# Kernel optimization log

Hardware: AMD Instinct MI355X
Metric: run time of the kernel (lower is better)

The kernel has to match this reference:

```python
import jax, jax.numpy as jnp
import numpy as np

L = 2048  # episode_len
B = 64    # batch
K = 256   # key_size
V = 256   # value_size
H = 8     # num_head


def setup_inputs() -> dict:
    key = jax.random.key(0)
    ks = jax.random.split(key, 9)
    query = jax.random.normal(ks[0], (B, K), dtype=jnp.float32)
    keys = jax.random.normal(ks[1], (L, B, K), dtype=jnp.float32)
    vals = jax.random.normal(ks[2], (L, B, V), dtype=jnp.float32)
    rpe_mod = jax.random.uniform(ks[3], (L, B, 1), dtype=jnp.float32)
    Wq = jax.random.normal(ks[4], (K, H * K), dtype=jnp.float32) * (1.0 / np.sqrt(K))
    bq = jnp.zeros((H * K,), dtype=jnp.float32)
    Wa = jax.random.normal(ks[5], (H * V, V), dtype=jnp.float32) * (1.0 / np.sqrt(H * V))
    ba = jnp.zeros((V,), dtype=jnp.float32)
    # per-sample valid length in [1, L] (nonzero so the softmax is well-defined,
    # matching read()'s early-return guard for empty memories)
    steps = jax.random.randint(ks[6], (B,), 1, L + 1, dtype=jnp.int32)
    return {"query": query, "keys": keys, "vals": vals, "rpe_mod": rpe_mod,
            "Wq": Wq, "bq": bq, "Wa": Wa, "ba": ba, "steps": steps}


def reference(query, keys, vals, rpe_mod, Wq, bq, Wa, ba, steps):
    # query encoder: [B,K] -> [B,H,K]
    q = (query @ Wq + bq).reshape(B, H, K)
    # RPE-modulated keys: [L,B,K]
    mod_keys = keys * rpe_mod
    # scores[l,b,h] = <mod_keys[l,b,:], q[b,h,:]>
    scores = jnp.einsum('lbk,bhk->lbh', mod_keys, q)
    # mask out positions >= steps[b] (equivalent to slicing keys[:step[i], i])
    valid = (jnp.arange(L, dtype=jnp.int32)[:, None] < steps[None, :])  # [L,B]
    scores = jnp.where(valid[:, :, None], scores, -jnp.inf)
    weight = jax.nn.softmax(scores, axis=0)  # softmax over stored steps
    # weighted memory read: [B,H,V]
    read = jnp.einsum('lbh,lbv->bhv', weight, vals)
    # head aggregation: [B, H*V] -> [B, V]
    out = read.reshape(B, H * V) @ Wa + ba
    return out
```

## Files before the change

### kernel.cpp

```cpp
#include <hip/hip_runtime.h>
#include <hip/hip_bf16.h>
#include <cstdint>

#define Ln 2048
#define Bn 64
#define Kd 256
#define Vd 256
#define Hn 8

#define CH 64
#define NCH 32

using u32 = unsigned int;
using u16 = unsigned short;

__device__ __forceinline__ float bflo(u32 u) { return __uint_as_float(u << 16); }
__device__ __forceinline__ float bfhi(u32 u) { return __uint_as_float(u & 0xffff0000u); }
__device__ __forceinline__ float bf1(u16 s) { return __uint_as_float(((u32)s) << 16); }
__device__ __forceinline__ float dot4(float4 a, float4 b) {
  return a.x * b.x + a.y * b.y + a.z * b.z + a.w * b.w;
}

__device__ __forceinline__ bool sniff_bf16(const void* keys) {
  const u16* q = (const u16*)keys;
  int lane = threadIdx.x & 63;
  u16 u = q[2 * (lane * 127)];
  u32 e = (u >> 7) & 0xff;
  bool sane = (u == 0) || (e >= 100 && e <= 134);
  return __popcll(__ballot(sane)) > 32;
}

__global__ __launch_bounds__(256) void k_prep(const void* keys, const void* query,
                                              const void* Wq, const void* bq,
                                              float* q_ws) {
  const bool bf = sniff_bf16(keys);
  const int t = threadIdx.x;
  const int chunk = blockIdx.x;
  const int b = blockIdx.y;

  __shared__ float ql[256];
  ql[t] = bf ? bf1(((const u16*)query)[b * 256 + t]) : ((const float*)query)[b * 256 + t];
  __syncthreads();

  int c0 = chunk * 512 + 2 * t;
  float a0, a1;
  if (bf) { a0 = bf1(((const u16*)bq)[c0]); a1 = bf1(((const u16*)bq)[c0 + 1]); }
  else    { a0 = ((const float*)bq)[c0];    a1 = ((const float*)bq)[c0 + 1]; }

  if (bf) {
    const u32* w = (const u32*)Wq + chunk * 256 + t;
    for (int k0 = 0; k0 < 256; k0 += 16) {
      u32 wv[16];
#pragma unroll
      for (int j = 0; j < 16; j++) wv[j] = w[(size_t)(k0 + j) * 1024];
#pragma unroll
      for (int j = 0; j < 16; j++) {
        float qk = ql[k0 + j];
        a0 += qk * bflo(wv[j]); a1 += qk * bfhi(wv[j]);
      }
    }
  } else {
    const float2* w = (const float2*)Wq + chunk * 256 + t;
    for (int k0 = 0; k0 < 256; k0 += 16) {
      float2 wv[16];
#pragma unroll
      for (int j = 0; j < 16; j++) wv[j] = w[(size_t)(k0 + j) * 1024];
#pragma unroll
      for (int j = 0; j < 16; j++) {
        float qk = ql[k0 + j];
        a0 += qk * wv[j].x; a1 += qk * wv[j].y;
      }
    }
  }
  q_ws[b * 2048 + c0] = a0;
  q_ws[b * 2048 + c0 + 1] = a1;
}

__global__ __launch_bounds__(256) void k_fused(const void* keys, const void* vals,
                                               const void* rpe, const int* steps,
                                               const float* q_ws, float* O_part,
                                               float2* mz_part) {
  const int b = blockIdx.y, chunk = blockIdx.x;
  const int lstart = chunk * CH;
  const int stepb = steps[b];
  if (lstart >= stepb) return;
  const int lcnt = min(CH, stepb - lstart);
  const bool bf = sniff_bf16(keys);
  const int t = threadIdx.x;
  const int lane = t & 63;
  const int wave = __builtin_amdgcn_readfirstlane(t >> 6);

  __shared__ __align__(16) float q_lds[Hn * Kd];
  __shared__ __align__(16) float w_lds[CH * 12];
  __shared__ float rpe_lds[CH];
  __shared__ float2 mz_lds[8];

  const int r8 = lane >> 3, ks8 = lane & 7;

#define LOAD_K(P, BB)                                                         \
  float4 P##0, P##1, P##2, P##3, P##4, P##5, P##6, P##7;                      \
  do {                                                                        \
    const int row_ = (BB) * 32 + wave * 8 + r8;                               \
    if (bf) {                                                                 \
      const u16* kb = (const u16*)keys +                                      \
          ((size_t)(lstart + row_) * 64 + b) * 256 + ks8 * 4;                 \
      uint2 u0 = *(const uint2*)(kb + 0);   uint2 u1 = *(const uint2*)(kb + 32);  \
      uint2 u2 = *(const uint2*)(kb + 64);  uint2 u3 = *(const uint2*)(kb + 96);  \
      uint2 u4 = *(const uint2*)(kb + 128); uint2 u5 = *(const uint2*)(kb + 160); \
      uint2 u6 = *(const uint2*)(kb + 192); uint2 u7 = *(const uint2*)(kb + 224); \
      P##0 = make_float4(bflo(u0.x), bfhi(u0.x), bflo(u0.y), bfhi(u0.y));     \
      P##1 = make_float4(bflo(u1.x), bfhi(u1.x), bflo(u1.y), bfhi(u1.y));     \
      P##2 = make_float4(bflo(u2.x), bfhi(u2.x), bflo(u2.y), bfhi(u2.y));     \
      P##3 = make_float4(bflo(u3.x), bfhi(u3.x), bflo(u3.y), bfhi(u3.y));     \
      P##4 = make_float4(bflo(u4.x), bfhi(u4.x), bflo(u4.y), bfhi(u4.y));     \
      P##5 = make_float4(bflo(u5.x), bfhi(u5.x), bflo(u5.y), bfhi(u5.y));     \
      P##6 = make_float4(bflo(u6.x), bfhi(u6.x), bflo(u6.y), bfhi(u6.y));     \
      P##7 = make_float4(bflo(u7.x), bfhi(u7.x), bflo(u7.y), bfhi(u7.y));     \
    } else {                                                                  \
      const float* kb = (const float*)keys +                                  \
          ((size_t)(lstart + row_) * 64 + b) * 256 + ks8 * 4;                 \
      P##0 = *(const float4*)(kb + 0);   P##1 = *(const float4*)(kb + 32);    \
      P##2 = *(const float4*)(kb + 64);  P##3 = *(const float4*)(kb + 96);    \
      P##4 = *(const float4*)(kb + 128); P##5 = *(const float4*)(kb + 160);   \
      P##6 = *(const float4*)(kb + 192); P##7 = *(const float4*)(kb + 224);   \
    }                                                                         \
  } while (0)

#define QF(H, J) (*(const float4*)(qp + (H) * 256 + (J) * 32))
#define SCH(P, H)                                                             \
  (dot4(P##0, QF(H, 0)) + dot4(P##1, QF(H, 1)) + dot4(P##2, QF(H, 2)) +       \
   dot4(P##3, QF(H, 3)) + dot4(P##4, QF(H, 4)) + dot4(P##5, QF(H, 5)) +       \
   dot4(P##6, QF(H, 6)) + dot4(P##7, QF(H, 7)))
#define R3(A)                                                                 \
  A += __shfl_xor(A, 1); A += __shfl_xor(A, 2); A += __shfl_xor(A, 4);

#define COMPUTE_WRITE(P, BB) do {                                             \
    const int row_ = (BB) * 32 + wave * 8 + r8;                               \
    float a0 = SCH(P, 0), a1 = SCH(P, 1), a2 = SCH(P, 2), a3 = SCH(P, 3);     \
    float a4 = SCH(P, 4), a5 = SCH(P, 5), a6 = SCH(P, 6), a7 = SCH(P, 7);     \
    R3(a0) R3(a1) R3(a2) R3(a3) R3(a4) R3(a5) R3(a6) R3(a7)                   \
    if (ks8 == 0) {                                                           \
      float rp = rpe_lds[row_];                                               \
      w_lds[row_ * 12 + 0] = a0 * rp; w_lds[row_ * 12 + 1] = a1 * rp;         \
      w_lds[row_ * 12 + 2] = a2 * rp; w_lds[row_ * 12 + 3] = a3 * rp;         \
      w_lds[row_ * 12 + 4] = a4 * rp; w_lds[row_ * 12 + 5] = a5 * rp;         \
      w_lds[row_ * 12 + 6] = a6 * rp; w_lds[row_ * 12 + 7] = a7 * rp;         \
    }                                                                         \
  } while (0)

  LOAD_K(p, 0);

  {
    const float4* src = (const float4*)(q_ws + (size_t)b * 2048) + t * 2;
    float4 f0 = src[0], f1 = src[1];
    *((float4*)q_lds + t * 2) = f0;
    *((float4*)q_lds + t * 2 + 1) = f1;
  }
  if (t < CH) {
    int l = lstart + t;
    rpe_lds[t] = bf ? bf1(((const u16*)rpe)[l * 64 + b]) : ((const float*)rpe)[l * 64 + b];
  }
  __syncthreads();

  const float* qp = q_lds + ks8 * 4;

  LOAD_K(s, 1);
  COMPUTE_WRITE(p, 0);
  COMPUTE_WRITE(s, 1);
  __syncthreads();

  {
    const int h = t >> 5, j = t & 31;
    float s0 = (j < lcnt) ? w_lds[j * 12 + h] : -3.0e38f;
    float s1 = (j + 32 < lcnt) ? w_lds[(j + 32) * 12 + h] : -3.0e38f;
    float m = fmaxf(s0, s1);
#pragma unroll
    for (int off = 16; off >= 1; off >>= 1) m = fmaxf(m, __shfl_xor(m, off, 32));
    float e0 = (j < lcnt) ? __expf(s0 - m) : 0.f;
    float e1 = (j + 32 < lcnt) ? __expf(s1 - m) : 0.f;
    w_lds[j * 12 + h] = e0;
    w_lds[(j + 32) * 12 + h] = e1;
    float zs = e0 + e1;
#pragma unroll
    for (int off = 16; off >= 1; off >>= 1) zs += __shfl_xor(zs, off, 32);
    if (j == 0) mz_lds[h] = make_float2(m, zs);
  }
  __syncthreads();
  if (t < 8) mz_part[((size_t)chunk * 64 + b) * 8 + t] = mz_lds[t];

  const int vslot = lane & 15, rg = lane >> 4;
  float acc[8][4];
#pragma unroll
  for (int hh = 0; hh < 8; hh++)
#pragma unroll
    for (int cc = 0; cc < 4; cc++) acc[hh][cc] = 0.f;

  if (bf) {
    const u32* vb = (const u32*)vals + ((size_t)lstart * 64 + b) * 128 + wave * 32 + vslot * 2;
    for (int i0 = 0; i0 < 16; i0 += 8) {
      uint2 uu[8];
#pragma unroll
      for (int jb = 0; jb < 8; jb++) {
        int row = rg + 4 * (i0 + jb);
        uu[jb] = *(const uint2*)(vb + (size_t)row * 8192);
      }
#pragma unroll
      for (int jb = 0; jb < 8; jb++) {
        int row = rg + 4 * (i0 + jb);
        float4 w0 = *(const float4*)&w_lds[row * 12];
        float4 w1 = *(const float4*)&w_lds[row * 12 + 4];
        float v0 = bflo(uu[jb].x), v1 = bfhi(uu[jb].x);
        float v2 = bflo(uu[jb].y), v3 = bfhi(uu[jb].y);
        acc[0][0] += w0.x * v0; acc[0][1] += w0.x * v1; acc[0][2] += w0.x * v2; acc[0][3] += w0.x * v3;
        acc[1][0] += w0.y * v0; acc[1][1] += w0.y * v1; acc[1][2] += w0.y * v2; acc[1][3] += w0.y * v3;
        acc[2][0] += w0.z * v0; acc[2][1] += w0.z * v1; acc[2][2] += w0.z * v2; acc[2][3] += w0.z * v3;
        acc[3][0] += w0.w * v0; acc[3][1] += w0.w * v1; acc[3][2] += w0.w * v2; acc[3][3] += w0.w * v3;
        acc[4][0] += w1.x * v0; acc[4][1] += w1.x * v1; acc[4][2] += w1.x * v2; acc[4][3] += w1.x * v3;
        acc[5][0] += w1.y * v0; acc[5][1] += w1.y * v1; acc[5][2] += w1.y * v2; acc[5][3] += w1.y * v3;
        acc[6][0] += w1.z * v0; acc[6][1] += w1.z * v1; acc[6][2] += w1.z * v2; acc[6][3] += w1.z * v3;
        acc[7][0] += w1.w * v0; acc[7][1] += w1.w * v1; acc[7][2] += w1.w * v2; acc[7][3] += w1.w * v3;
      }
    }
  } else {
    const float* vb = (const float*)vals + ((size_t)lstart * 64 + b) * 256 + wave * 64 + vslot * 4;
    for (int i0 = 0; i0 < 16; i0 += 8) {
      float4 vv[8];
#pragma unroll
      for (int jb = 0; jb < 8; jb++) {
        int row = rg + 4 * (i0 + jb);
        vv[jb] = *(const float4*)(vb + (size_t)row * 16384);
      }
#pragma unroll
      for (int jb = 0; jb < 8; jb++) {
        int row = rg + 4 * (i0 + jb);
        float4 w0 = *(const float4*)&w_lds[row * 12];
        float4 w1 = *(const float4*)&w_lds[row * 12 + 4];
        acc[0][0] += w0.x * vv[jb].x; acc[0][1] += w0.x * vv[jb].y; acc[0][2] += w0.x * vv[jb].z; acc[0][3] += w0.x * vv[jb].w;
        acc[1][0] += w0.y * vv[jb].x; acc[1][1] += w0.y * vv[jb].y; acc[1][2] += w0.y * vv[jb].z; acc[1][3] += w0.y * vv[jb].w;
        acc[2][0] += w0.z * vv[jb].x; acc[2][1] += w0.z * vv[jb].y; acc[2][2] += w0.z * vv[jb].z; acc[2][3] += w0.z * vv[jb].w;
        acc[3][0] += w0.w * vv[jb].x; acc[3][1] += w0.w * vv[jb].y; acc[3][2] += w0.w * vv[jb].z; acc[3][3] += w0.w * vv[jb].w;
        acc[4][0] += w1.x * vv[jb].x; acc[4][1] += w1.x * vv[jb].y; acc[4][2] += w1.x * vv[jb].z; acc[4][3] += w1.x * vv[jb].w;
        acc[5][0] += w1.y * vv[jb].x; acc[5][1] += w1.y * vv[jb].y; acc[5][2] += w1.y * vv[jb].z; acc[5][3] += w1.y * vv[jb].w;
        acc[6][0] += w1.z * vv[jb].x; acc[6][1] += w1.z * vv[jb].y; acc[6][2] += w1.z * vv[jb].z; acc[6][3] += w1.z * vv[jb].w;
        acc[7][0] += w1.w * vv[jb].x; acc[7][1] += w1.w * vv[jb].y; acc[7][2] += w1.w * vv[jb].z; acc[7][3] += w1.w * vv[jb].w;
      }
    }
  }

#pragma unroll
  for (int hh = 0; hh < 8; hh++)
#pragma unroll
    for (int cc = 0; cc < 4; cc++) {
      float v = acc[hh][cc];
      v += __shfl_xor(v, 16);
      v += __shfl_xor(v, 32);
      acc[hh][cc] = v;
    }
  if (rg == 0) {
    float* op = O_part + ((size_t)chunk * 64 + b) * 2048 + wave * 64 + vslot * 4;
#pragma unroll
    for (int hh = 0; hh < 8; hh++) {
      float4 o = make_float4(acc[hh][0], acc[hh][1], acc[hh][2], acc[hh][3]);
      *(float4*)&op[hh * 256] = o;
    }
  }
}

__global__ __launch_bounds__(256) void k_out1(const void* keys, const void* Wa,
                                              const int* steps, const float* O_part,
                                              const float2* mz_part, float* out_part) {
  const int h = blockIdx.x, b = blockIdx.y;
  const bool bf = sniff_bf16(keys);
  const int t = threadIdx.x;
  const int nlive = (steps[b] + CH - 1) >> 6;

  float2 mzv[NCH];
#pragma unroll
  for (int c = 0; c < NCH; c++)
    mzv[c] = (c < nlive) ? mz_part[((size_t)c * 64 + b) * 8 + h] : make_float2(-3.0e38f, 0.f);
  float M = -3.0e38f;
#pragma unroll
  for (int c = 0; c < NCH; c++) M = fmaxf(M, mzv[c].x);
  float sc[NCH];
  float Z = 0.f;
#pragma unroll
  for (int c = 0; c < NCH; c++) {
    sc[c] = __expf(mzv[c].x - M);
    Z += sc[c] * mzv[c].y;
  }
  const float zi = 1.0f / Z;

  __shared__ float rn[256];
  {
    const float* op = O_part + (size_t)b * 2048 + h * 256 + t;
    float s = 0.f;
    float ov[16];
#pragma unroll
    for (int c = 0; c < 16; c++) ov[c] = (c < nlive) ? op[(size_t)c * 131072] : 0.f;
#pragma unroll
    for (int c = 0; c < 16; c++) s += sc[c] * ov[c];
#pragma unroll
    for (int c = 0; c < 16; c++) ov[c] = (c + 16 < nlive) ? op[(size_t)(c + 16) * 131072] : 0.f;
#pragma unroll
    for (int c = 0; c < 16; c++) s += sc[c + 16] * ov[c];
    rn[t] = s * zi;
  }
  __syncthreads();

  float a = 0.f;
  if (bf) {
    const u32* wa = (const u32*)Wa + (size_t)(h * 256) * 128 + (t >> 1);
    const bool hi = (t & 1);
    for (int c0 = 0; c0 < 256; c0 += 16) {
      u32 wv[16];
#pragma unroll
      for (int j = 0; j < 16; j++) wv[j] = wa[(size_t)(c0 + j) * 128];
#pragma unroll
      for (int j = 0; j < 16; j++)
        a += rn[c0 + j] * (hi ? bfhi(wv[j]) : bflo(wv[j]));
    }
  } else {
    const float* wa = (const float*)Wa + (size_t)(h * 256) * 256 + t;
    for (int c0 = 0; c0 < 256; c0 += 16) {
      float wv[16];
#pragma unroll
      for (int j = 0; j < 16; j++) wv[j] = wa[(size_t)(c0 + j) * 256];
#pragma unroll
      for (int j = 0; j < 16; j++) a += rn[c0 + j] * wv[j];
    }
  }
  out_part[(size_t)(h * 64 + b) * 256 + t] = a;
}

__global__ __launch_bounds__(256) void k_out2(const void* keys, const void* ba,
                                              const float* out_part, void* out) {
  const int b = blockIdx.x, t = threadIdx.x;
  const bool bf = sniff_bf16(keys);
  float s = bf ? bf1(((const u16*)ba)[t]) : ((const float*)ba)[t];
  float ov[8];
#pragma unroll
  for (int h = 0; h < 8; h++) ov[h] = out_part[(size_t)(h * 64 + b) * 256 + t];
#pragma unroll
  for (int h = 0; h < 8; h++) s += ov[h];
  if (bf)
    ((__hip_bfloat16*)out)[b * 256 + t] = __float2bfloat16(s);
  else
    ((float*)out)[b * 256 + t] = s;
}

extern "C" void kernel_launch(void* const* d_in, const int* in_sizes, int n_in,
                              void* d_out, int out_size, void* d_ws, size_t ws_size,
                              hipStream_t stream) {
  (void)in_sizes; (void)n_in; (void)out_size; (void)ws_size;
  const void* query = d_in[0];
  const void* keys = d_in[1];
  const void* vals = d_in[2];
  const void* rpe = d_in[3];
  const void* Wq = d_in[4];
  const void* bq = d_in[5];
  const void* Wa = d_in[6];
  const void* ba = d_in[7];
  const int* steps = (const int*)d_in[8];

  float* ws = (float*)d_ws;
  float* q_ws = ws;
  float* O_part = ws + 131072;
  float2* mz_part = (float2*)(ws + 131072 + 4194304);
  float* out_part = ws + 131072 + 4194304 + 32768;

  k_prep<<<dim3(4, 64), 256, 0, stream>>>(keys, query, Wq, bq, q_ws);
  k_fused<<<dim3(NCH, 64), 256, 0, stream>>>(keys, vals, rpe, steps, q_ws, O_part, mz_part);
  k_out1<<<dim3(8, 64), 256, 0, stream>>>(keys, Wa, steps, O_part, mz_part, out_part);
  k_out2<<<64, 256, 0, stream>>>(keys, ba, out_part, d_out);
}
```

Measured before the change: 315.8 us.

## Make fused attention kernel persistent over strided chunks with software-pipelined key loads

The fused score/softmax/read kernel now launches 8 blocks per batch row instead of one per 64-step chunk. Each block loops over every eighth chunk, starting at an offset rotated by the batch index. The query vector is staged into LDS once per block rather than once per chunk. The next chunk's keys, the first half of the current chunk's values and the rpe factors are loaded ahead of the barriers, to overlap memory latency with the score and softmax work. The cost is fewer resident blocks, so less parallelism to hide latency, plus higher register pressure from the extra in-flight key and value buffers.

```diff
diff --git a/kernel.cpp b/kernel.cpp
--- a/kernel.cpp
+++ b/kernel.cpp
@@ -80,49 +80,46 @@
                                                const void* rpe, const int* steps,
                                                const float* q_ws, float* O_part,
                                                float2* mz_part) {
-  const int b = blockIdx.y, chunk = blockIdx.x;
-  const int lstart = chunk * CH;
+  const int b = blockIdx.y;
   const int stepb = steps[b];
-  if (lstart >= stepb) return;
-  const int lcnt = min(CH, stepb - lstart);
+  const int g = (blockIdx.x + b) & 7;
+  if (g * CH >= stepb) return;
   const bool bf = sniff_bf16(keys);
   const int t = threadIdx.x;
   const int lane = t & 63;
   const int wave = __builtin_amdgcn_readfirstlane(t >> 6);
 
+  const int r8 = lane >> 3, ks8 = lane & 7;
+  const int vslot = lane & 15, rg = lane >> 4;
+  const int jj = t & 31, hh8 = t >> 5;
+
   __shared__ __align__(16) float q_lds[Hn * Kd];
   __shared__ __align__(16) float w_lds[CH * 12];
-  __shared__ float rpe_lds[CH];
-  __shared__ float2 mz_lds[8];
-
-  const int r8 = lane >> 3, ks8 = lane & 7;
-
-#define LOAD_K(P, BB)                                                         \
-  float4 P##0, P##1, P##2, P##3, P##4, P##5, P##6, P##7;                      \
-  do {                                                                        \
-    const int row_ = (BB) * 32 + wave * 8 + r8;                               \
+
+  float4 p0, p1, p2, p3, p4, p5, p6, p7;
+  float4 n0, n1, n2, n3, n4, n5, n6, n7;
+
+#define ASSIGN_K(P, LROW) do {                                                \
     if (bf) {                                                                 \
-      const u16* kb = (const u16*)keys +                                      \
-          ((size_t)(lstart + row_) * 64 + b) * 256 + ks8 * 4;                 \
-      uint2 u0 = *(const uint2*)(kb + 0);   uint2 u1 = *(const uint2*)(kb + 32);  \
-      uint2 u2 = *(const uint2*)(kb + 64);  uint2 u3 = *(const uint2*)(kb + 96);  \
-      uint2 u4 = *(const uint2*)(kb + 128); uint2 u5 = *(const uint2*)(kb + 160); \
-      uint2 u6 = *(const uint2*)(kb + 192); uint2 u7 = *(const uint2*)(kb + 224); \
-      P##0 = make_float4(bflo(u0.x), bfhi(u0.x), bflo(u0.y), bfhi(u0.y));     \
-      P##1 = make_float4(bflo(u1.x), bfhi(u1.x), bflo(u1.y), bfhi(u1.y));     \
-      P##2 = make_float4(bflo(u2.x), bfhi(u2.x), bflo(u2.y), bfhi(u2.y));     \
-      P##3 = make_float4(bflo(u3.x), bfhi(u3.x), bflo(u3.y), bfhi(u3.y));     \
-      P##4 = make_float4(bflo(u4.x), bfhi(u4.x), bflo(u4.y), bfhi(u4.y));     \
-      P##5 = make_float4(bflo(u5.x), bfhi(u5.x), bflo(u5.y), bfhi(u5.y));     \
-      P##6 = make_float4(bflo(u6.x), bfhi(u6.x), bflo(u6.y), bfhi(u6.y));     \
-      P##7 = make_float4(bflo(u7.x), bfhi(u7.x), bflo(u7.y), bfhi(u7.y));     \
+      const u16* kb_ = (const u16*)keys + ((size_t)(LROW) * 64 + b) * 256 + ks8 * 4; \
+      uint2 u0_ = *(const uint2*)(kb_ + 0);   uint2 u1_ = *(const uint2*)(kb_ + 32);  \
+      uint2 u2_ = *(const uint2*)(kb_ + 64);  uint2 u3_ = *(const uint2*)(kb_ + 96);  \
+      uint2 u4_ = *(const uint2*)(kb_ + 128); uint2 u5_ = *(const uint2*)(kb_ + 160); \
+      uint2 u6_ = *(const uint2*)(kb_ + 192); uint2 u7_ = *(const uint2*)(kb_ + 224); \
+      P##0 = make_float4(bflo(u0_.x), bfhi(u0_.x), bflo(u0_.y), bfhi(u0_.y)); \
+      P##1 = make_float4(bflo(u1_.x), bfhi(u1_.x), bflo(u1_.y), bfhi(u1_.y)); \
+      P##2 = make_float4(bflo(u2_.x), bfhi(u2_.x), bflo(u2_.y), bfhi(u2_.y)); \
+      P##3 = make_float4(bflo(u3_.x), bfhi(u3_.x), bflo(u3_.y), bfhi(u3_.y)); \
+      P##4 = make_float4(bflo(u4_.x), bfhi(u4_.x), bflo(u4_.y), bfhi(u4_.y)); \
+      P##5 = make_float4(bflo(u5_.x), bfhi(u5_.x), bflo(u5_.y), bfhi(u5_.y)); \
+      P##6 = make_float4(bflo(u6_.x), bfhi(u6_.x), bflo(u6_.y), bfhi(u6_.y)); \
+      P##7 = make_float4(bflo(u7_.x), bfhi(u7_.x), bflo(u7_.y), bfhi(u7_.y)); \
     } else {                                                                  \
-      const float* kb = (const float*)keys +                                  \
-          ((size_t)(lstart + row_) * 64 + b) * 256 + ks8 * 4;                 \
-      P##0 = *(const float4*)(kb + 0);   P##1 = *(const float4*)(kb + 32);    \
-      P##2 = *(const float4*)(kb + 64);  P##3 = *(const float4*)(kb + 96);    \
-      P##4 = *(const float4*)(kb + 128); P##5 = *(const float4*)(kb + 160);   \
-      P##6 = *(const float4*)(kb + 192); P##7 = *(const float4*)(kb + 224);   \
+      const float* kb_ = (const float*)keys + ((size_t)(LROW) * 64 + b) * 256 + ks8 * 4; \
+      P##0 = *(const float4*)(kb_ + 0);   P##1 = *(const float4*)(kb_ + 32);  \
+      P##2 = *(const float4*)(kb_ + 64);  P##3 = *(const float4*)(kb_ + 96);  \
+      P##4 = *(const float4*)(kb_ + 128); P##5 = *(const float4*)(kb_ + 160); \
+      P##6 = *(const float4*)(kb_ + 192); P##7 = *(const float4*)(kb_ + 224); \
     }                                                                         \
   } while (0)
 
@@ -134,135 +131,168 @@
 #define R3(A)                                                                 \
   A += __shfl_xor(A, 1); A += __shfl_xor(A, 2); A += __shfl_xor(A, 4);
 
-#define COMPUTE_WRITE(P, BB) do {                                             \
-    const int row_ = (BB) * 32 + wave * 8 + r8;                               \
+#define COMPUTE_WRITE(P, BOFF) do {                                           \
+    const int row_ = (BOFF) + wave * 8 + r8;                                  \
     float a0 = SCH(P, 0), a1 = SCH(P, 1), a2 = SCH(P, 2), a3 = SCH(P, 3);     \
     float a4 = SCH(P, 4), a5 = SCH(P, 5), a6 = SCH(P, 6), a7 = SCH(P, 7);     \
     R3(a0) R3(a1) R3(a2) R3(a3) R3(a4) R3(a5) R3(a6) R3(a7)                   \
     if (ks8 == 0) {                                                           \
-      float rp = rpe_lds[row_];                                               \
-      w_lds[row_ * 12 + 0] = a0 * rp; w_lds[row_ * 12 + 1] = a1 * rp;         \
-      w_lds[row_ * 12 + 2] = a2 * rp; w_lds[row_ * 12 + 3] = a3 * rp;         \
-      w_lds[row_ * 12 + 4] = a4 * rp; w_lds[row_ * 12 + 5] = a5 * rp;         \
-      w_lds[row_ * 12 + 6] = a6 * rp; w_lds[row_ * 12 + 7] = a7 * rp;         \
+      w_lds[row_ * 12 + 0] = a0; w_lds[row_ * 12 + 1] = a1;                   \
+      w_lds[row_ * 12 + 2] = a2; w_lds[row_ * 12 + 3] = a3;                   \
+      w_lds[row_ * 12 + 4] = a4; w_lds[row_ * 12 + 5] = a5;                   \
+      w_lds[row_ * 12 + 6] = a6; w_lds[row_ * 12 + 7] = a7;                   \
     }                                                                         \
   } while (0)
 
-  LOAD_K(p, 0);
-
+  int c = g;
+  int ls = c * CH;
+
+  ASSIGN_K(p, ls + wave * 8 + r8);
   {
     const float4* src = (const float4*)(q_ws + (size_t)b * 2048) + t * 2;
     float4 f0 = src[0], f1 = src[1];
     *((float4*)q_lds + t * 2) = f0;
     *((float4*)q_lds + t * 2 + 1) = f1;
   }
-  if (t < CH) {
-    int l = lstart + t;
-    rpe_lds[t] = bf ? bf1(((const u16*)rpe)[l * 64 + b]) : ((const float*)rpe)[l * 64 + b];
-  }
   __syncthreads();
 
   const float* qp = q_lds + ks8 * 4;
 
-  LOAD_K(s, 1);
-  COMPUTE_WRITE(p, 0);
-  COMPUTE_WRITE(s, 1);
-  __syncthreads();
-
-  {
-    const int h = t >> 5, j = t & 31;
-    float s0 = (j < lcnt) ? w_lds[j * 12 + h] : -3.0e38f;
-    float s1 = (j + 32 < lcnt) ? w_lds[(j + 32) * 12 + h] : -3.0e38f;
-    float m = fmaxf(s0, s1);
-#pragma unroll
-    for (int off = 16; off >= 1; off >>= 1) m = fmaxf(m, __shfl_xor(m, off, 32));
-    float e0 = (j < lcnt) ? __expf(s0 - m) : 0.f;
-    float e1 = (j + 32 < lcnt) ? __expf(s1 - m) : 0.f;
-    w_lds[j * 12 + h] = e0;
-    w_lds[(j + 32) * 12 + h] = e1;
-    float zs = e0 + e1;
-#pragma unroll
-    for (int off = 16; off >= 1; off >>= 1) zs += __shfl_xor(zs, off, 32);
-    if (j == 0) mz_lds[h] = make_float2(m, zs);
-  }
-  __syncthreads();
-  if (t < 8) mz_part[((size_t)chunk * 64 + b) * 8 + t] = mz_lds[t];
-
-  const int vslot = lane & 15, rg = lane >> 4;
-  float acc[8][4];
-#pragma unroll
-  for (int hh = 0; hh < 8; hh++)
-#pragma unroll
-    for (int cc = 0; cc < 4; cc++) acc[hh][cc] = 0.f;
-
-  if (bf) {
-    const u32* vb = (const u32*)vals + ((size_t)lstart * 64 + b) * 128 + wave * 32 + vslot * 2;
-    for (int i0 = 0; i0 < 16; i0 += 8) {
-      uint2 uu[8];
+  for (;;) {
+    const int lcnt = min(CH, stepb - ls);
+    const bool lastc = (c + 8 >= NCH) || ((c + 8) * CH >= stepb);
+
+    float rpA, rpB;
+    if (bf) {
+      rpA = bf1(((const u16*)rpe)[(size_t)(ls + jj) * 64 + b]);
+      rpB = bf1(((const u16*)rpe)[(size_t)(ls + jj + 32) * 64 + b]);
+    } else {
+      rpA = ((const float*)rpe)[(size_t)(ls + jj) * 64 + b];
+      rpB = ((const float*)rpe)[(size_t)(ls + jj + 32) * 64 + b];
+    }
+
+    ASSIGN_K(n, ls + 32 + wave * 8 + r8);
+    COMPUTE_WRITE(p, 0);
+    COMPUTE_WRITE(n, 32);
+
+    float4 va[8];
+    const float* vbf = (const float*)vals + ((size_t)ls * 64 + b) * 256 + wave * 64 + vslot * 4;
+    if (!bf) {
+#pragma unroll
+      for (int jb = 0; jb < 8; jb++)
+        va[jb] = *(const float4*)(vbf + (size_t)(rg + 4 * jb) * 16384);
+    }
+    if (!lastc) ASSIGN_K(p, ls + 512 + wave * 8 + r8);
+    __syncthreads();
+
+    {
+      float s0 = (jj < lcnt) ? w_lds[jj * 12 + hh8] * rpA : -3.0e38f;
+      float s1 = (jj + 32 < lcnt) ? w_lds[(jj + 32) * 12 + hh8] * rpB : -3.0e38f;
+      float m = fmaxf(s0, s1);
+#pragma unroll
+      for (int off = 16; off >= 1; off >>= 1) m = fmaxf(m, __shfl_xor(m, off, 32));
+      float e0 = (jj < lcnt) ? __expf(s0 - m) : 0.f;
+      float e1 = (jj + 32 < lcnt) ? __expf(s1 - m) : 0.f;
+      w_lds[jj * 12 + hh8] = e0;
+      w_lds[(jj + 32) * 12 + hh8] = e1;
+      float zs = e0 + e1;
+#pragma unroll
+      for (int off = 16; off >= 1; off >>= 1) zs += __shfl_xor(zs, off, 32);
+      if (jj == 0) mz_part[((size_t)c * 64 + b) * 8 + hh8] = make_float2(m, zs);
+    }
+    __syncthreads();
+
+    float acc[8][4];
+#pragma unroll
+    for (int hh = 0; hh < 8; hh++)
+#pragma unroll
+      for (int cc = 0; cc < 4; cc++) acc[hh][cc] = 0.f;
+
+    if (bf) {
+      const u32* vb = (const u32*)vals + ((size_t)ls * 64 + b) * 128 + wave * 32 + vslot * 2;
+      for (int i0 = 0; i0 < 16; i0 += 8) {
+        uint2 uu[8];
+#pragma unroll
+        for (int jb = 0; jb < 8; jb++) {
+          int row = rg + 4 * (i0 + jb);
+          uu[jb] = *(const uint2*)(vb + (size_t)row * 8192);
+        }
+#pragma unroll
+        for (int jb = 0; jb < 8; jb++) {
+          int row = rg + 4 * (i0 + jb);
+          float4 w0 = *(const float4*)&w_lds[row * 12];
+          float4 w1 = *(const float4*)&w_lds[row * 12 + 4];
+          float v0 = bflo(uu[jb].x), v1 = bfhi(uu[jb].x);
+          float v2 = bflo(uu[jb].y), v3 = bfhi(uu[jb].y);
+          acc[0][0] += w0.x * v0; acc[0][1] += w0.x * v1; acc[0][2] += w0.x * v2; acc[0][3] += w0.x * v3;
+          acc[1][0] += w0.y * v0; acc[1][1] += w0.y * v1; acc[1][2] += w0.y * v2; acc[1][3] += w0.y * v3;
+          acc[2][0] += w0.z * v0; acc[2][1] += w0.z * v1; acc[2][2] += w0.z * v2; acc[2][3] += w0.z * v3;
+          acc[3][0] += w0.w * v0; acc[3][1] += w0.w * v1; acc[3][2] += w0.w * v2; acc[3][3] += w0.w * v3;
+          acc[4][0] += w1.x * v0; acc[4][1] += w1.x * v1; acc[4][2] += w1.x * v2; acc[4][3] += w1.x * v3;
+          acc[5][0] += w1.y * v0; acc[5][1] += w1.y * v1; acc[5][2] += w1.y * v2; acc[5][3] += w1.y * v3;
+          acc[6][0] += w1.z * v0; acc[6][1] += w1.z * v1; acc[6][2] += w1.z * v2; acc[6][3] += w1.z * v3;
+          acc[7][0] += w1.w * v0; acc[7][1] += w1.w * v1; acc[7][2] += w1.w * v2; acc[7][3] += w1.w * v3;
+        }
+      }
+    } else {
+      float4 vbb[8];
+#pragma unroll
+      for (int jb = 0; jb < 8; jb++)
+        vbb[jb] = *(const float4*)(vbf + (size_t)(rg + 4 * (8 + jb)) * 16384);
 #pragma unroll
       for (int jb = 0; jb < 8; jb++) {
-        int row = rg + 4 * (i0 + jb);
-        uu[jb] = *(const uint2*)(vb + (size_t)row * 8192);
-      }
-#pragma unroll
-      for (int jb = 0; jb < 8; jb++) {
-        int row = rg + 4 * (i0 + jb);
+        int row = rg + 4 * jb;
         float4 w0 = *(const float4*)&w_lds[row * 12];
         float4 w1 = *(const float4*)&w_lds[row * 12 + 4];
-        float v0 = bflo(uu[jb].x), v1 = bfhi(uu[jb].x);
-        float v2 = bflo(uu[jb].y), v3 = bfhi(uu[jb].y);
-        acc[0][0] += w0.x * v0; acc[0][1] += w0.x * v1; acc[0][2] += w0.x * v2; acc[0][3] += w0.x * v3;
-        acc[1][0] += w0.y * v0; acc[1][1] += w0.y * v1; acc[1][2] += w0.y * v2; acc[1][3] += w0.y * v3;
-        acc[2][0] += w0.z * v0; acc[2][1] += w0.z * v1; acc[2][2] += w0.z * v2; acc[2][3] += w0.z * v3;
-        acc[3][0] += w0.w * v0; acc[3][1] += w0.w * v1; acc[3][2] += w0.w * v2; acc[3][3] += w0.w * v3;
-        acc[4][0] += w1.x * v0; acc[4][1] += w1.x * v1; acc[4][2] += w1.x * v2; acc[4][3] += w1.x * v3;
-        acc[5][0] += w1.y * v0; acc[5][1] += w1.y * v1; acc[5][2] += w1.y * v2; acc[5][3] += w1.y * v3;
-        acc[6][0] += w1.z * v0; acc[6][1] += w1.z * v1; acc[6][2] += w1.z * v2; acc[6][3] += w1.z * v3;
-        acc[7][0] += w1.w * v0; acc[7][1] += w1.w * v1; acc[7][2] += w1.w * v2; acc[7][3] += w1.w * v3;
-      }
-    }
-  } else {
-    const float* vb = (const float*)vals + ((size_t)lstart * 64 + b) * 256 + wave * 64 + vslot * 4;
-    for (int i0 = 0; i0 < 16; i0 += 8) {
-      float4 vv[8];
+        float4 vv = va[jb];
+        acc[0][0] += w0.x * vv.x; acc[0][1] += w0.x * vv.y; acc[0][2] += w0.x * vv.z; acc[0][3] += w0.x * vv.w;
+        acc[1][0] += w0.y * vv.x; acc[1][1] += w0.y * vv.y; acc[1][2] += w0.y * vv.z; acc[1][3] += w0.y * vv.w;
+        acc[2][0] += w0.z * vv.x; acc[2][1] += w0.z * vv.y; acc[2][2] += w0.z * vv.z; acc[2][3] += w0.z * vv.w;
+        acc[3][0] += w0.w * vv.x; acc[3][1] += w0.w * vv.y; acc[3][2] += w0.w * vv.z; acc[3][3] += w0.w * vv.w;
+        acc[4][0] += w1.x * vv.x; acc[4][1] += w1.x * vv.y; acc[4][2] += w1.x * vv.z; acc[4][3] += w1.x * vv.w;
+        acc[5][0] += w1.y * vv.x; acc[5][1] += w1.y * vv.y; acc[5][2] += w1.y * vv.z; acc[5][3] += w1.y * vv.w;
+        acc[6][0] += w1.z * vv.x; acc[6][1] += w1.z * vv.y; acc[6][2] += w1.z * vv.z; acc[6][3] += w1.z * vv.w;
+        acc[7][0] += w1.w * vv.x; acc[7][1] += w1.w * vv.y; acc[7][2] += w1.w * vv.z; acc[7][3] += w1.w * vv.w;
+      }
 #pragma unroll
       for (int jb = 0; jb < 8; jb++) {
-        int row = rg + 4 * (i0 + jb);
-        vv[jb] = *(const float4*)(vb + (size_t)row * 16384);
-      }
-#pragma unroll
-      for (int jb = 0; jb < 8; jb++) {
-        int row = rg + 4 * (i0 + jb);
+        int row = rg + 4 * (8 + jb);
         float4 w0 = *(const float4*)&w_lds[row * 12];
         float4 w1 = *(const float4*)&w_lds[row * 12 + 4];
-        acc[0][0] += w0.x * vv[jb].x; acc[0][1] += w0.x * vv[jb].y; acc[0][2] += w0.x * vv[jb].z; acc[0][3] += w0.x * vv[jb].w;
-        acc[1][0] += w0.y * vv[jb].x; acc[1][1] += w0.y * vv[jb].y; acc[1][2] += w0.y * vv[jb].z; acc[1][3] += w0.y * vv[jb].w;
-        acc[2][0] += w0.z * vv[jb].x; acc[2][1] += w0.z * vv[jb].y; acc[2][2] += w0.z * vv[jb].z; acc[2][3] += w0.z * vv[jb].w;
-        acc[3][0] += w0.w * vv[jb].x; acc[3][1] += w0.w * vv[jb].y; acc[3][2] += w0.w * vv[jb].z; acc[3][3] += w0.w * vv[jb].w;
-        acc[4][0] += w1.x * vv[jb].x; acc[4][1] += w1.x * vv[jb].y; acc[4][2] += w1.x * vv[jb].z; acc[4][3] += w1.x * vv[jb].w;
-        acc[5][0] += w1.y * vv[jb].x; acc[5][1] += w1.y * vv[jb].y; acc[5][2] += w1.y * vv[jb].z; acc[5][3] += w1.y * vv[jb].w;
-        acc[6][0] += w1.z * vv[jb].x; acc[6][1] += w1.z * vv[jb].y; acc[6][2] += w1.z * vv[jb].z; acc[6][3] += w1.z * vv[jb].w;
-        acc[7][0] += w1.w * vv[jb].x; acc[7][1] += w1.w * vv[jb].y; acc[7][2] += w1.w * vv[jb].z; acc[7][3] += w1.w * vv[jb].w;
-      }
-    }
-  }
-
-#pragma unroll
-  for (int hh = 0; hh < 8; hh++)
-#pragma unroll
-    for (int cc = 0; cc < 4; cc++) {
-      float v = acc[hh][cc];
-      v += __shfl_xor(v, 16);
-      v += __shfl_xor(v, 32);
-      acc[hh][cc] = v;
-    }
-  if (rg == 0) {
-    float* op = O_part + ((size_t)chunk * 64 + b) * 2048 + wave * 64 + vslot * 4;
-#pragma unroll
-    for (int hh = 0; hh < 8; hh++) {
-      float4 o = make_float4(acc[hh][0], acc[hh][1], acc[hh][2], acc[hh][3]);
-      *(float4*)&op[hh * 256] = o;
-    }
+        float4 vv = vbb[jb];
+        acc[0][0] += w0.x * vv.x; acc[0][1] += w0.x * vv.y; acc[0][2] += w0.x * vv.z; acc[0][3] += w0.x * vv.w;
+        acc[1][0] += w0.y * vv.x; acc[1][1] += w0.y * vv.y; acc[1][2] += w0.y * vv.z; acc[1][3] += w0.y * vv.w;
+        acc[2][0] += w0.z * vv.x; acc[2][1] += w0.z * vv.y; acc[2][2] += w0.z * vv.z; acc[2][3] += w0.z * vv.w;
+        acc[3][0] += w0.w * vv.x; acc[3][1] += w0.w * vv.y; acc[3][2] += w0.w * vv.z; acc[3][3] += w0.w * vv.w;
+        acc[4][0] += w1.x * vv.x; acc[4][1] += w1.x * vv.y; acc[4][2] += w1.x * vv.z; acc[4][3] += w1.x * vv.w;
+        acc[5][0] += w1.y * vv.x; acc[5][1] += w1.y * vv.y; acc[5][2] += w1.y * vv.z; acc[5][3] += w1.y * vv.w;
+        acc[6][0] += w1.z * vv.x; acc[6][1] += w1.z * vv.y; acc[6][2] += w1.z * vv.z; acc[6][3] += w1.z * vv.w;
+        acc[7][0] += w1.w * vv.x; acc[7][1] += w1.w * vv.y; acc[7][2] += w1.w * vv.z; acc[7][3] += w1.w * vv.w;
+      }
+    }
+
+#pragma unroll
+    for (int hh = 0; hh < 8; hh++)
+#pragma unroll
+      for (int cc = 0; cc < 4; cc++) {
+        float v = acc[hh][cc];
+        v += __shfl_xor(v, 16);
+        v += __shfl_xor(v, 32);
+        acc[hh][cc] = v;
+      }
+    if (rg == 0) {
+      float* op = O_part + ((size_t)c * 64 + b) * 2048 + wave * 64 + vslot * 4;
+#pragma unroll
+      for (int hh = 0; hh < 8; hh++) {
+        float4 o = make_float4(acc[hh][0], acc[hh][1], acc[hh][2], acc[hh][3]);
+        *(float4*)&op[hh * 256] = o;
+      }
+    }
+
+    if (lastc) break;
+    __syncthreads();
+    c += 8;
+    ls += 512;
   }
 }
 
@@ -369,7 +399,7 @@
   float* out_part = ws + 131072 + 4194304 + 32768;
 
   k_prep<<<dim3(4, 64), 256, 0, stream>>>(keys, query, Wq, bq, q_ws);
-  k_fused<<<dim3(NCH, 64), 256, 0, stream>>>(keys, vals, rpe, steps, q_ws, O_part, mz_part);
+  k_fused<<<dim3(8, 64), 256, 0, stream>>>(keys, vals, rpe, steps, q_ws, O_part, mz_part);
   k_out1<<<dim3(8, 64), 256, 0, stream>>>(keys, Wa, steps, O_part, mz_part, out_part);
   k_out2<<<64, 256, 0, stream>>>(keys, ba, out_part, d_out);
 }
```

Result: faster. 302.7 us (-4.2%).
